# Performance work log

Measured on AMD Instinct MI355X. Metric: run time of the kernel, lower is better.

The kernel has to match this reference:

```python
import jax, jax.numpy as jnp
import numpy as np


def _largest_component_mask(fg):
    # fg: (B,H,W) bool foreground mask. Returns bool mask of the largest
    # 8-connected component per batch element (skimage.measure.label default
    # connectivity for 2D is 8-connectivity).
    B, H, W = fg.shape
    HW = H * W
    big = jnp.int32(HW)  # sentinel label for background / padding
    idx = jnp.arange(HW, dtype=jnp.int32).reshape(1, H, W)
    l0 = jnp.broadcast_to(idx, (B, H, W))

    def neighbor_min(l):
        lm = jnp.where(fg, l, big)
        p = jnp.pad(lm, ((0, 0), (1, 1), (1, 1)), constant_values=HW)
        m = lm
        for di in (-1, 0, 1):
            for dj in (-1, 0, 1):
                if di == 0 and dj == 0:
                    continue
                m = jnp.minimum(m, p[:, 1 + di:1 + di + H, 1 + dj:1 + dj + W])
        return m

    def body(carry):
        l, _ = carry
        # one step of label propagation (min over 8-neighborhood, fg only)
        l2 = jnp.where(fg, jnp.minimum(l, neighbor_min(l)), l)
        # pointer jumping: l <- l[l]  (labels are in-row linear indices)
        lf = l2.reshape(B, HW)
        l2 = jnp.take_along_axis(lf, lf, axis=1).reshape(B, H, W)
        return l2, jnp.any(l2 != l)

    l, _ = jax.lax.while_loop(lambda c: c[1], body, (l0, jnp.bool_(True)))

    lf = l.reshape(B, HW)
    w = fg.reshape(B, HW).astype(jnp.float32)
    counts = jax.vmap(lambda li, wi: jnp.bincount(li, weights=wi, length=HW))(lf, w)
    largest = jnp.argmax(counts, axis=1).astype(jnp.int32)  # (B,) root label of biggest cc
    return (l == largest[:, None, None]) & fg


def setup_inputs() -> dict:
    key = jax.random.key(0)
    x = jax.random.normal(key, (16, 2, 1024, 1024), dtype=jnp.float32)
    return {"x": x}


def reference(x):
    # binary segmentation = argmax over class dim; background class = 0
    binary = jnp.argmax(x, axis=1)          # (B,H,W) int
    fg = binary > 0
    mask = _largest_component_mask(fg)       # (B,H,W) bool, largest cc only
    return x * mask[:, None, :, :].astype(x.dtype)
```

## Files before the change

kernel.cpp:

```cpp
#include <hip/hip_runtime.h>
#include <stdint.h>

static constexpr int BATCH = 16;
static constexpr int Hh = 1024;
static constexpr int Ww = 1024;
static constexpr int HW = Hh * Ww;
static constexpr int NPIX = BATCH * HW;
static constexpr int TS = 64;
static constexpr int TILES_PER_IMG = (Hh / TS) * (Ww / TS);
static constexpr int NODES = TS * 32;

static constexpr int CAPB = 65536;
static constexpr int NB1  = CAPB / 1024;


__device__ __forceinline__ int find_root_halve(int* parent, int i) {
    while (true) {
        int p = parent[i];
        if (p == i) return i;
        int gp = parent[p];
        if (gp == p) return p;
        parent[i] = gp;
        i = gp;
    }
}

__device__ __forceinline__ int find_root_ro(const int* parent, int i) {
    int p = parent[i];
    while (p != i) { i = p; p = parent[i]; }
    return i;
}

__device__ __forceinline__ void merge_uf(int* parent, int a, int b) {
    while (true) {
        a = find_root_halve(parent, a);
        b = find_root_halve(parent, b);
        if (a == b) return;
        if (a > b) { int t = a; a = b; b = t; }
        int old = atomicMin(&parent[b], a);
        if (old == b) return;
        b = old;
    }
}


__global__ __launch_bounds__(256) void k_local(const float* __restrict__ x,
                                               int* __restrict__ parent,
                                               int* __restrict__ counts,
                                               unsigned long long* __restrict__ list,
                                               unsigned* __restrict__ nlist) {
    __shared__ int lab[NODES];
    __shared__ int cnt[NODES];
    __shared__ unsigned char runpos[NODES];
    __shared__ unsigned long long rowmask[TS];
    __shared__ int wbase[4];
    __shared__ int blkbase;

    int tile = blockIdx.x;
    int b = tile >> 8;
    int t = tile & 255;
    int th = t >> 4, tw = t & 15;
    int h0 = th * TS, w0 = tw * TS;
    const float* xb = x + (size_t)b * 2 * (size_t)HW;
    int base = b * HW + h0 * Ww + w0;
    int wv = threadIdx.x >> 6;
    int lane = threadIdx.x & 63;
    unsigned long long below = (lane == 0) ? 0ull : ((1ull << lane) - 1);

    #pragma unroll
    for (int k = 0; k < NODES / 256; k++) {
        int i = threadIdx.x + k * 256;
        lab[i] = i;
        cnt[i] = 0;
    }

    #pragma unroll
    for (int k = 0; k < TS / 4; k++) {
        int r = (k << 2) | wv;
        int off = (h0 + r) * Ww + w0 + lane;
        float x0 = xb[off];
        float x1 = xb[off + HW];
        bool fg = x1 > x0;
        unsigned long long m = __ballot(fg);
        if (lane == 0) rowmask[r] = m;
        unsigned long long rs = m & ~(m << 1);
        if ((rs >> lane) & 1) {
            int node = (r << 5) | (int)__popcll(rs & below);
            runpos[node] = (unsigned char)lane;
        }
    }
    __syncthreads();

    auto find_lh = [&](int i) {
        while (true) {
            int p = lab[i];
            if (p == i) return i;
            int gp = lab[p];
            if (gp == p) return p;
            lab[i] = gp;
            i = gp;
        }
    };
    auto merge_l = [&](int a, int c) {
        while (true) {
            a = find_lh(a); c = find_lh(c);
            if (a == c) return;
            if (a > c) { int tt = a; a = c; c = tt; }
            int old = atomicMin(&lab[c], a);
            if (old == c) return;
            c = old;
        }
    };

    for (int k = 0; k < TS / 4; k++) {
        int r = (k << 2) | wv;
        if (r == 0) continue;
        unsigned long long m = rowmask[r];
        bool fg = (m >> lane) & 1;
        if (!fg) continue;
        unsigned long long mu = rowmask[r - 1];
        unsigned long long rs = m & ~(m << 1);
        unsigned long long rsu = mu & ~(mu << 1);
        unsigned long long zb = ~m & below;
        int b0 = zb ? (64 - __clzll(zb)) : 0;
        int n0 = (r << 5) | (int)__popcll(rs & ((b0 == 0) ? 0ull : ((1ull << b0) - 1)));
        bool upC = (mu >> lane) & 1;
        bool upL = (lane > 0)  && ((mu >> (lane - 1)) & 1);
        bool upR = (lane < 63) && ((mu >> (lane + 1)) & 1);
        bool atStart = (lane == b0);
        bool atEnd = (lane == 63) || !((m >> (lane + 1)) & 1);
        auto unode = [&](int lu) {
            unsigned long long belu = (lu == 0) ? 0ull : ((1ull << lu) - 1);
            unsigned long long zbu = ~mu & belu;
            int u0 = zbu ? (64 - __clzll(zbu)) : 0;
            return ((r - 1) << 5) | (int)__popcll(rsu & ((u0 == 0) ? 0ull : ((1ull << u0) - 1)));
        };
        if (upC && (atStart || !upL)) merge_l(n0, unode(lane));
        if (atStart && !upC && upL)   merge_l(n0, unode(lane - 1));
        if (atEnd && !upC && upR)     merge_l(n0, unode(lane + 1));
    }
    __syncthreads();

    for (int k = 0; k < TS / 4; k++) {
        int r = (k << 2) | wv;
        unsigned long long m = rowmask[r];
        unsigned long long rs = m & ~(m << 1);
        bool need = (rs >> lane) & 1;
        int root = 0, len = 0;
        if (need) {
            int node = (r << 5) | (int)__popcll(rs & below);
            unsigned long long za = (~m) >> lane;
            len = za ? (int)(__ffsll(za) - 1) : (64 - lane);
            root = node;
            { int q = lab[root]; while (q != root) { root = q; q = lab[root]; } }
            if (root != node) lab[node] = root;
        }
        while (__any(need)) {
            unsigned long long bm = __ballot(need);
            int src = (int)(__ffsll(bm) - 1);
            int rr = __shfl(root, src);
            bool mine = need && (root == rr);
            int v = mine ? len : 0;
            #pragma unroll
            for (int off = 32; off > 0; off >>= 1) v += __shfl_xor(v, off);
            if (lane == src) atomicAdd(&cnt[rr], v);
            if (mine) need = false;
        }
    }
    __syncthreads();

    #pragma unroll
    for (int k = 0; k < TS / 4; k++) {
        int r = (k << 2) | wv;
        unsigned long long m = rowmask[r];
        unsigned long long rs = m & ~(m << 1);
        bool fg = (m >> lane) & 1;
        int g = base + r * Ww + lane;
        int pv = -1;
        if (fg) {
            unsigned long long zb = ~m & below;
            int b0 = zb ? (64 - __clzll(zb)) : 0;
            int node = (r << 5) | (int)__popcll(rs & ((b0 == 0) ? 0ull : ((1ull << b0) - 1)));
            int root = lab[node];
            pv = base + (root >> 5) * Ww + (int)runpos[root];
        }
        parent[g] = pv;
    }

    int wtot = 0;
    unsigned rootbits = 0;
    #pragma unroll
    for (int k = 0; k < NODES / 256; k++) {
        int node = (k << 8) | threadIdx.x;
        bool isr = cnt[node] > 0;
        if (isr) rootbits |= (1u << k);
        unsigned long long bm = __ballot(isr);
        wtot += (int)__popcll(bm);
    }
    if (lane == 0) wbase[wv] = wtot;
    __syncthreads();
    if (threadIdx.x == 0) {
        int s0 = wbase[0], s1 = wbase[1], s2 = wbase[2], s3 = wbase[3];
        blkbase = (int)atomicAdd(&nlist[b << 5], (unsigned)(s0 + s1 + s2 + s3));
        wbase[0] = 0; wbase[1] = s0; wbase[2] = s0 + s1; wbase[3] = s0 + s1 + s2;
    }
    __syncthreads();
    int woff = blkbase + wbase[wv];
    #pragma unroll
    for (int k = 0; k < NODES / 256; k++) {
        bool isr = (rootbits >> k) & 1;
        unsigned long long bm = __ballot(isr);
        if (isr) {
            int slot = woff + (int)__popcll(bm & below);
            if (slot < CAPB) {
                int node = (k << 8) | threadIdx.x;
                int g = base + (node >> 5) * Ww + (int)runpos[node];
                list[(size_t)b * CAPB + slot] =
                    (((unsigned long long)(unsigned)cnt[node]) << 32) |
                    (unsigned long long)(0xFFFFFFFFu - (unsigned)g);
                counts[g] = 0;
            }
        }
        woff += (int)__popcll(bm);
    }
}


static constexpr int BORDER_A = (Hh / TS) * Ww;
static constexpr int BORDER_PER_B = BORDER_A + Hh * (Ww / TS) * 2;

__global__ __launch_bounds__(256) void k_border(int* __restrict__ parent) {
    int b = blockIdx.y;
    int t = blockIdx.x * blockDim.x + threadIdx.x;
    int h, w;
    if (t < BORDER_A) {
        h = (t >> 10) << 6;
        w = t & 1023;
    } else {
        int t2 = t - BORDER_A;
        int c = t2 & 31;
        h = t2 >> 5;
        w = ((c >> 1) << 6) + ((c & 1) ? (TS - 1) : 0);
    }
    int i = b * HW + h * Ww + w;
    if (parent[i] < 0) return;
    bool hb = (h & (TS - 1)) == 0;
    bool wb = (w & (TS - 1)) == 0;
    bool we = (w & (TS - 1)) == (TS - 1);
    if (wb && w > 0 && parent[i - 1] >= 0) merge_uf(parent, i, i - 1);
    if (h > 0) {
        if (hb && parent[i - Ww] >= 0) merge_uf(parent, i, i - Ww);
        if ((hb | wb) && w > 0 && parent[i - Ww - 1] >= 0) merge_uf(parent, i, i - Ww - 1);
        if ((hb | we) && w < Ww - 1 && parent[i - Ww + 1] >= 0) merge_uf(parent, i, i - Ww + 1);
    }
}


__global__ __launch_bounds__(256) void k_roots(int* __restrict__ parent,
                                               int* __restrict__ counts,
                                               unsigned long long* __restrict__ list,
                                               const unsigned* __restrict__ nlist) {
    int b = blockIdx.y;
    int n = (int)nlist[b << 5]; if (n > CAPB) n = CAPB;
    int j = blockIdx.x * 256 + threadIdx.x;
    bool need = j < n;
    int r = 0, c = 0;
    size_t idx = (size_t)b * CAPB + j;
    if (need) {
        unsigned long long e = list[idx];
        int g = (int)(0xFFFFFFFFu - (unsigned)(e & 0xFFFFFFFFull));
        c = (int)(e >> 32);
        r = find_root_ro(parent, g);
        if (r != g) parent[g] = r;
        list[idx] = (unsigned long long)(0xFFFFFFFFu - (unsigned)r);
    }
    int lane = threadIdx.x & 63;
    while (__any(need)) {
        unsigned long long bm = __ballot(need);
        int src = (int)(__ffsll(bm) - 1);
        int rr = __shfl(r, src);
        bool mine = need && (r == rr);
        int v = mine ? c : 0;
        #pragma unroll
        for (int off = 32; off > 0; off >>= 1) v += __shfl_xor(v, off);
        if (lane == src) atomicAdd(&counts[rr], v);
        if (mine) need = false;
    }
}


__global__ __launch_bounds__(256) void k_argmax1(const unsigned long long* __restrict__ list,
                                                 const int* __restrict__ counts,
                                                 const unsigned* __restrict__ nlist,
                                                 unsigned long long* __restrict__ blockmax) {
    int b = blockIdx.y;
    int n = (int)nlist[b << 5]; if (n > CAPB) n = CAPB;
    unsigned long long v = 0ull;
    #pragma unroll
    for (int k = 0; k < 4; k++) {
        int j = blockIdx.x * 1024 + k * 256 + threadIdx.x;
        if (j < n) {
            unsigned rinv = (unsigned)(list[(size_t)b * CAPB + j] & 0xFFFFFFFFull);
            int r = (int)(0xFFFFFFFFu - rinv);
            int c = counts[r];
            unsigned long long o =
                (((unsigned long long)(unsigned)c) << 32) | (unsigned long long)rinv;
            if (o > v) v = o;
        }
    }
    for (int off = 32; off > 0; off >>= 1) {
        unsigned long long o = __shfl_down(v, off);
        if (o > v) v = o;
    }
    __shared__ unsigned long long sm[4];
    if ((threadIdx.x & 63) == 0) sm[threadIdx.x >> 6] = v;
    __syncthreads();
    if (threadIdx.x == 0) {
        v = sm[0];
        #pragma unroll
        for (int w = 1; w < 4; w++) if (sm[w] > v) v = sm[w];
        blockmax[b * NB1 + blockIdx.x] = v;
    }
}


__global__ __launch_bounds__(256) void k_argmax2(const unsigned long long* __restrict__ blockmax,
                                                 unsigned long long* __restrict__ best) {
    int b = blockIdx.x;
    unsigned long long v = 0ull;
    if (threadIdx.x < NB1) v = blockmax[b * NB1 + threadIdx.x];
    for (int off = 32; off > 0; off >>= 1) {
        unsigned long long o = __shfl_down(v, off);
        if (o > v) v = o;
    }
    __shared__ unsigned long long sm[4];
    if ((threadIdx.x & 63) == 0) sm[threadIdx.x >> 6] = v;
    __syncthreads();
    if (threadIdx.x == 0) {
        v = sm[0];
        #pragma unroll
        for (int w = 1; w < 4; w++) if (sm[w] > v) v = sm[w];
        best[b] = v;
    }
}


__global__ __launch_bounds__(256) void k_final(const float* __restrict__ x,
                                               const int* __restrict__ parent,
                                               const unsigned long long* __restrict__ best,
                                               float* __restrict__ out) {
    int i = blockIdx.x * blockDim.x + threadIdx.x;
    int b = i >> 20;
    int p = i & (HW - 1);
    unsigned long long bv = best[b];
    int broot = (int)(0xFFFFFFFFu - (unsigned)(bv & 0xFFFFFFFFull));
    int pr = parent[i];
    int a = (pr >= 0) ? pr : 0;
    int root = parent[a];
    bool mask = (pr >= 0) && (root == broot);
    const float* xb = x + ((size_t)b * 2) * (size_t)HW;
    float* ob = out + ((size_t)b * 2) * (size_t)HW;
    float x0 = xb[p];
    float x1 = xb[p + HW];
    ob[p]      = mask ? x0 : 0.0f;
    ob[p + HW] = mask ? x1 : 0.0f;
}


extern "C" void kernel_launch(void* const* d_in, const int* in_sizes, int n_in,
                              void* d_out, int out_size, void* d_ws, size_t ws_size,
                              hipStream_t stream) {
    const float* x = (const float*)d_in[0];
    float* out = (float*)d_out;

    unsigned long long* best = (unsigned long long*)d_ws;
    unsigned* nlist = (unsigned*)((char*)d_ws + 256);
    int* parent = (int*)((char*)d_ws + 4096);
    int* counts = parent + NPIX;
    unsigned long long* blockmax = (unsigned long long*)(counts + NPIX);
    unsigned long long* list = blockmax + 1024;

    dim3 blk(256);
    dim3 grd(NPIX / 256);
    dim3 grd_tiles(BATCH * TILES_PER_IMG);
    dim3 grd_border(BORDER_PER_B / 256, BATCH);
    dim3 grd_roots(CAPB / 256, BATCH);
    dim3 grd_arg1(NB1, BATCH);

    hipMemsetAsync(nlist, 0, 2048, stream);

    k_local   <<<grd_tiles, blk, 0, stream>>>(x, parent, counts, list, nlist);
    k_border  <<<grd_border, blk, 0, stream>>>(parent);
    k_roots   <<<grd_roots, blk, 0, stream>>>(parent, counts, list, nlist);
    k_argmax1 <<<grd_arg1, blk, 0, stream>>>(list, counts, nlist, blockmax);
    k_argmax2 <<<dim3(BATCH), blk, 0, stream>>>(blockmax, best);
    k_final   <<<grd, blk, 0, stream>>>(x, parent, best, out);
}
```

Before: 555.4 us.

## Run-based border merging, per-node count accumulation, and float4 vectorized final pass

Adds a per-run length table in shared memory so component sizes are accumulated per run node with direct shared atomics, replacing the wave-serialized ballot/shuffle reduction loop. Rewrites the tile-border merge kernel to work per wavefront on 64-pixel border segments, using ballots to merge only at run starts and ends instead of per-pixel merges. Vectorizes the final masking kernel to process four pixels per thread with float4/int4 loads and stores. The main risk is correctness of the border-merge coverage at tile corners and extra shared-atomic contention.

Measured after the change: 496.1 us. -10.7%, faster.

```diff
diff --git a/kernel.cpp b/kernel.cpp
--- a/kernel.cpp
+++ b/kernel.cpp
@@ -52,6 +52,7 @@
     __shared__ int lab[NODES];
     __shared__ int cnt[NODES];
     __shared__ unsigned char runpos[NODES];
+    __shared__ unsigned char runlen[NODES];
     __shared__ unsigned long long rowmask[TS];
     __shared__ int wbase[4];
     __shared__ int blkbase;
@@ -72,7 +73,9 @@
         int i = threadIdx.x + k * 256;
         lab[i] = i;
         cnt[i] = 0;
-    }
+        runlen[i] = 0;
+    }
+    __syncthreads();
 
     #pragma unroll
     for (int k = 0; k < TS / 4; k++) {
@@ -87,6 +90,8 @@
         if ((rs >> lane) & 1) {
             int node = (r << 5) | (int)__popcll(rs & below);
             runpos[node] = (unsigned char)lane;
+            unsigned long long za = (~m) >> lane;
+            runlen[node] = (unsigned char)(za ? (int)(__ffsll(za) - 1) : (64 - lane));
         }
     }
     __syncthreads();
@@ -141,30 +146,15 @@
     }
     __syncthreads();
 
-    for (int k = 0; k < TS / 4; k++) {
-        int r = (k << 2) | wv;
-        unsigned long long m = rowmask[r];
-        unsigned long long rs = m & ~(m << 1);
-        bool need = (rs >> lane) & 1;
-        int root = 0, len = 0;
-        if (need) {
-            int node = (r << 5) | (int)__popcll(rs & below);
-            unsigned long long za = (~m) >> lane;
-            len = za ? (int)(__ffsll(za) - 1) : (64 - lane);
-            root = node;
+    #pragma unroll
+    for (int k = 0; k < NODES / 256; k++) {
+        int node = (k << 8) | threadIdx.x;
+        int L = (int)runlen[node];
+        if (L > 0) {
+            int root = node;
             { int q = lab[root]; while (q != root) { root = q; q = lab[root]; } }
             if (root != node) lab[node] = root;
-        }
-        while (__any(need)) {
-            unsigned long long bm = __ballot(need);
-            int src = (int)(__ffsll(bm) - 1);
-            int rr = __shfl(root, src);
-            bool mine = need && (root == rr);
-            int v = mine ? len : 0;
-            #pragma unroll
-            for (int off = 32; off > 0; off >>= 1) v += __shfl_xor(v, off);
-            if (lane == src) atomicAdd(&cnt[rr], v);
-            if (mine) need = false;
+            atomicAdd(&cnt[root], L);
         }
     }
     __syncthreads();
@@ -226,32 +216,70 @@
 }
 
 
-static constexpr int BORDER_A = (Hh / TS) * Ww;
-static constexpr int BORDER_PER_B = BORDER_A + Hh * (Ww / TS) * 2;
-
 __global__ __launch_bounds__(256) void k_border(int* __restrict__ parent) {
     int b = blockIdx.y;
-    int t = blockIdx.x * blockDim.x + threadIdx.x;
-    int h, w;
-    if (t < BORDER_A) {
-        h = (t >> 10) << 6;
-        w = t & 1023;
+    int wid = (blockIdx.x << 2) | (threadIdx.x >> 6);
+    int lane = threadIdx.x & 63;
+    unsigned long long below = (lane == 0) ? 0ull : ((1ull << lane) - 1);
+    int bbase = b * HW;
+
+    if (wid < 240) {
+        int s = wid & 15, rb = wid >> 4;
+        int h = (rb + 1) << 6;
+        int w0s = s << 6;
+        int i  = bbase + h * Ww + w0s + lane;
+        int iu = i - Ww;
+        int pm = parent[i];
+        int pu = parent[iu];
+        unsigned long long mB = __ballot(pm >= 0);
+        unsigned long long mA = __ballot(pu >= 0);
+        if (pm >= 0) {
+            unsigned long long zb = ~mB & below;
+            int b0 = zb ? (64 - __clzll(zb)) : 0;
+            bool upC = (mA >> lane) & 1;
+            bool upL = (lane > 0)  && ((mA >> (lane - 1)) & 1);
+            bool upR = (lane < 63) && ((mA >> (lane + 1)) & 1);
+            bool atStart = (lane == b0);
+            bool atEnd = (lane == 63) || !((mB >> (lane + 1)) & 1);
+            if (upC && (atStart || !upL)) merge_uf(parent, i, iu);
+            if (atStart && !upC && upL)   merge_uf(parent, i, iu - 1);
+            if (atEnd && !upC && upR)     merge_uf(parent, i, iu + 1);
+        }
+        if (lane == 0 && w0s > 0) {
+            int pAp = parent[i - 1];
+            int pBp = parent[iu - 1];
+            if (pm >= 0 && pBp >= 0) merge_uf(parent, i, iu - 1);
+            if (pu >= 0 && pAp >= 0) merge_uf(parent, iu, i - 1);
+        }
     } else {
-        int t2 = t - BORDER_A;
-        int c = t2 & 31;
-        h = t2 >> 5;
-        w = ((c >> 1) << 6) + ((c & 1) ? (TS - 1) : 0);
-    }
-    int i = b * HW + h * Ww + w;
-    if (parent[i] < 0) return;
-    bool hb = (h & (TS - 1)) == 0;
-    bool wb = (w & (TS - 1)) == 0;
-    bool we = (w & (TS - 1)) == (TS - 1);
-    if (wb && w > 0 && parent[i - 1] >= 0) merge_uf(parent, i, i - 1);
-    if (h > 0) {
-        if (hb && parent[i - Ww] >= 0) merge_uf(parent, i, i - Ww);
-        if ((hb | wb) && w > 0 && parent[i - Ww - 1] >= 0) merge_uf(parent, i, i - Ww - 1);
-        if ((hb | we) && w < Ww - 1 && parent[i - Ww + 1] >= 0) merge_uf(parent, i, i - Ww + 1);
+        int wid2 = wid - 240;
+        int s = wid2 & 15, cb = wid2 >> 4;
+        int cR = (cb + 1) << 6;
+        int r = (s << 6) + lane;
+        int iR = bbase + r * Ww + cR;
+        int iL = iR - 1;
+        int pB = parent[iR];
+        int pA = parent[iL];
+        unsigned long long mB = __ballot(pB >= 0);
+        unsigned long long mA = __ballot(pA >= 0);
+        if (pB >= 0) {
+            unsigned long long zb = ~mB & below;
+            int b0 = zb ? (64 - __clzll(zb)) : 0;
+            bool upC = (mA >> lane) & 1;
+            bool upL = (lane > 0)  && ((mA >> (lane - 1)) & 1);
+            bool upR = (lane < 63) && ((mA >> (lane + 1)) & 1);
+            bool atStart = (lane == b0);
+            bool atEnd = (lane == 63) || !((mB >> (lane + 1)) & 1);
+            if (upC && (atStart || !upL)) merge_uf(parent, iR, iL);
+            if (atStart && !upC && upL)   merge_uf(parent, iR, iL - Ww);
+            if (atEnd && !upC && upR)     merge_uf(parent, iR, iL + Ww);
+        }
+        if (lane == 0 && s > 0) {
+            int aL = parent[iL - Ww];
+            int aR = parent[iR - Ww];
+            if (pB >= 0 && aL >= 0) merge_uf(parent, iR, iL - Ww);
+            if (pA >= 0 && aR >= 0) merge_uf(parent, iL, iR - Ww);
+        }
     }
 }
 
@@ -345,25 +373,36 @@
 }
 
 
-__global__ __launch_bounds__(256) void k_final(const float* __restrict__ x,
+__global__ __launch_bounds__(256) void k_final(const float4* __restrict__ x4,
+                                               const int4* __restrict__ parent4,
                                                const int* __restrict__ parent,
                                                const unsigned long long* __restrict__ best,
-                                               float* __restrict__ out) {
+                                               float4* __restrict__ out4) {
     int i = blockIdx.x * blockDim.x + threadIdx.x;
-    int b = i >> 20;
-    int p = i & (HW - 1);
+    int b = i >> 18;
+    int q = i & (HW / 4 - 1);
     unsigned long long bv = best[b];
     int broot = (int)(0xFFFFFFFFu - (unsigned)(bv & 0xFFFFFFFFull));
-    int pr = parent[i];
-    int a = (pr >= 0) ? pr : 0;
-    int root = parent[a];
-    bool mask = (pr >= 0) && (root == broot);
-    const float* xb = x + ((size_t)b * 2) * (size_t)HW;
-    float* ob = out + ((size_t)b * 2) * (size_t)HW;
-    float x0 = xb[p];
-    float x1 = xb[p + HW];
-    ob[p]      = mask ? x0 : 0.0f;
-    ob[p + HW] = mask ? x1 : 0.0f;
+    int4 pr = parent4[(size_t)b * (HW / 4) + q];
+    const float4* xb = x4 + (size_t)b * 2 * (HW / 4);
+    float4 x0 = xb[q];
+    float4 x1 = xb[q + HW / 4];
+    int a0 = pr.x >= 0 ? pr.x : 0;
+    int a1 = pr.y >= 0 ? pr.y : 0;
+    int a2 = pr.z >= 0 ? pr.z : 0;
+    int a3 = pr.w >= 0 ? pr.w : 0;
+    bool m0 = pr.x >= 0 && parent[a0] == broot;
+    bool m1 = pr.y >= 0 && parent[a1] == broot;
+    bool m2 = pr.z >= 0 && parent[a2] == broot;
+    bool m3 = pr.w >= 0 && parent[a3] == broot;
+    float4 o0, o1;
+    o0.x = m0 ? x0.x : 0.0f; o0.y = m1 ? x0.y : 0.0f;
+    o0.z = m2 ? x0.z : 0.0f; o0.w = m3 ? x0.w : 0.0f;
+    o1.x = m0 ? x1.x : 0.0f; o1.y = m1 ? x1.y : 0.0f;
+    o1.z = m2 ? x1.z : 0.0f; o1.w = m3 ? x1.w : 0.0f;
+    float4* ob = out4 + (size_t)b * 2 * (HW / 4);
+    ob[q]          = o0;
+    ob[q + HW / 4] = o1;
 }
 
 
@@ -381,11 +420,11 @@
     unsigned long long* list = blockmax + 1024;
 
     dim3 blk(256);
-    dim3 grd(NPIX / 256);
     dim3 grd_tiles(BATCH * TILES_PER_IMG);
-    dim3 grd_border(BORDER_PER_B / 256, BATCH);
+    dim3 grd_border(120, BATCH);
     dim3 grd_roots(CAPB / 256, BATCH);
     dim3 grd_arg1(NB1, BATCH);
+    dim3 grd_final(NPIX / 4 / 256);
 
     hipMemsetAsync(nlist, 0, 2048, stream);
 
@@ -394,5 +433,6 @@
     k_roots   <<<grd_roots, blk, 0, stream>>>(parent, counts, list, nlist);
     k_argmax1 <<<grd_arg1, blk, 0, stream>>>(list, counts, nlist, blockmax);
     k_argmax2 <<<dim3(BATCH), blk, 0, stream>>>(blockmax, best);
-    k_final   <<<grd, blk, 0, stream>>>(x, parent, best, out);
-}
+    k_final   <<<grd_final, blk, 0, stream>>>((const float4*)x, (const int4*)parent,
+                                              parent, best, (float4*)out);
+}
```
